# Kernel tuning notes

Hardware: AMD Instinct MI355X
Metric: run time of the kernel (lower is better)

The kernel has to match this reference:

```python
import jax, jax.numpy as jnp
import numpy as np

DIM = 1024
NUM_HEADS = 16
HEAD_DIM = DIM // NUM_HEADS


def _rope(x):
    # x: (B*H, L, hd). ESM-style rotary embedding with rotate_half.
    L, hd = x.shape[1], x.shape[2]
    inv_freq = 1.0 / (10000.0 ** (jnp.arange(0, hd, 2, dtype=jnp.float32) / hd))
    t = jnp.arange(L, dtype=jnp.float32)
    freqs = t[:, None] * inv_freq[None, :]          # (L, hd/2)
    emb = jnp.concatenate([freqs, freqs], axis=-1)   # (L, hd)
    cos, sin = jnp.cos(emb), jnp.sin(emb)
    x1, x2 = jnp.split(x, 2, axis=-1)
    rot = jnp.concatenate([-x2, x1], axis=-1)
    return x * cos + rot * sin


def setup_inputs() -> dict:
    key = jax.random.key(0)
    ks = jax.random.split(key, 10)
    L, N, D = 2048, 1, DIM
    query = jax.random.normal(ks[0], (L, N, D), dtype=jnp.float32)
    asym_ids = jnp.sort(jax.random.randint(ks[1], (N, L), 0, 4), axis=-1)
    s = 0.02
    wq = s * jax.random.normal(ks[2], (D, D), dtype=jnp.float32)
    wk = s * jax.random.normal(ks[3], (D, D), dtype=jnp.float32)
    wv = s * jax.random.normal(ks[4], (D, D), dtype=jnp.float32)
    wo = s * jax.random.normal(ks[5], (D, D), dtype=jnp.float32)
    bq = s * jax.random.normal(ks[6], (D,), dtype=jnp.float32)
    bk = s * jax.random.normal(ks[7], (D,), dtype=jnp.float32)
    bv = s * jax.random.normal(ks[8], (D,), dtype=jnp.float32)
    bo = s * jax.random.normal(ks[9], (D,), dtype=jnp.float32)
    return {"query": query, "asym_ids": asym_ids, "wq": wq, "bq": bq,
            "wk": wk, "bk": bk, "wv": wv, "bv": bv, "wo": wo, "bo": bo}


def reference(query, asym_ids, wq, bq, wk, bk, wv, bv, wo, bo):
    L, N, D = query.shape
    H, hd = NUM_HEADS, HEAD_DIM
    scaling = 1.0 / np.sqrt(hd)

    q = (query @ wq.T + bq) * scaling
    k = query @ wk.T + bk
    v = query @ wv.T + bv

    def to_bh(x):  # (L, N, D) -> (N*H, L, hd)
        return x.reshape(L, N * H, hd).transpose(1, 0, 2)

    q, k, v = to_bh(q), to_bh(k), to_bh(v)

    # raw scores (pre-RoPE), rpe scores (post-RoPE)
    raw = jnp.einsum('ble,bme->blm', q, k).reshape(N, H, L, L)
    qr, kr = _rope(q), _rope(k)
    rpe = jnp.einsum('ble,bme->blm', qr, kr).reshape(N, H, L, L)

    avg = jnp.mean(rpe - raw, axis=(0, 1), keepdims=True)          # (1,1,L,L)
    asym_mask = asym_ids[:, :, None] == asym_ids[:, None, :]        # (N,L,L)
    attn_weights = jnp.where(asym_mask[:, None], rpe, raw + avg)    # (N,H,L,L)

    probs = jax.nn.softmax(attn_weights, axis=-1)
    attn = jnp.einsum('nhlm,nhme->nhle', probs, v.reshape(N, H, L, hd))
    attn = attn.transpose(2, 0, 1, 3).reshape(L, N, D)
    out = attn @ wo.T + bo
    attn_weights_avg = jnp.mean(probs, axis=1)  # (N, L, L)
    return out, attn_weights_avg
```

## Files before the change

### kernel.cpp

```cpp
#include <hip/hip_runtime.h>

#define L 2048
#define D 1024
#define NH 16
#define HD 64
#define SPLIT 4
#define JCH (L / SPLIT)
#define LOG2E 1.4426950408889634f

typedef __attribute__((ext_vector_type(8))) short bf16x8;
typedef __attribute__((ext_vector_type(4))) float f32x4;

#define MFMA(a, b, c) __builtin_amdgcn_mfma_f32_16x16x32_bf16(a, b, c, 0, 0, 0)

__device__ __forceinline__ short f2bf(float x) {
  unsigned u = __float_as_uint(x);
  u = (u + 0x7FFFu + ((u >> 16) & 1u)) >> 16;
  return (short)u;
}

__device__ __forceinline__ void gll16(const void* g, void* l) {
  __builtin_amdgcn_global_load_lds(
      (const __attribute__((address_space(1))) void*)(uintptr_t)g,
      (__attribute__((address_space(3))) void*)(unsigned)(uintptr_t)l, 16, 0, 0);
}

__global__ void trig_kernel(float* __restrict__ costab, float* __restrict__ sintab) {
  int idx = blockIdx.x * blockDim.x + threadIdx.x;
  int t = idx >> 5, fi = idx & 31;
  float f = exp2f(-(float)fi * (13.287712379549449f / 32.0f));
  float ang = (float)t * f;
  costab[idx] = cosf(ang);
  sintab[idx] = sinf(ang);
}

__global__ void f2bf4_kernel(const float* __restrict__ in, short* __restrict__ out, int n4) {
  int i = blockIdx.x * blockDim.x + threadIdx.x;
  if (i < n4) {
    float4 v = ((const float4*)in)[i];
    short4 o;
    o.x = f2bf(v.x); o.y = f2bf(v.y); o.z = f2bf(v.z); o.w = f2bf(v.w);
    ((short4*)out)[i] = o;
  }
}

__global__ __launch_bounds__(256) void proj_kernel(
    const short* __restrict__ X, const short* __restrict__ W,
    const float* __restrict__ bias, const float* __restrict__ costab,
    const float* __restrict__ sintab, int mode,
    short* __restrict__ out_main, short* __restrict__ out_rope) {
  int w = threadIdx.x >> 6, lane = threadIdx.x & 63;
  int c = lane & 15, g = lane >> 4;
  int wi0 = blockIdx.y * 128 + (w >> 1) * 64;
  int wj0 = blockIdx.x * 128 + (w & 1) * 64;

  f32x4 acc[4][4];
#pragma unroll
  for (int m = 0; m < 4; ++m)
#pragma unroll
    for (int n = 0; n < 4; ++n) acc[m][n] = (f32x4){0.f, 0.f, 0.f, 0.f};

  for (int k0 = 0; k0 < D; k0 += 32) {
    bf16x8 aF[4], bF[4];
#pragma unroll
    for (int m = 0; m < 4; ++m)
      aF[m] = *(const bf16x8*)(X + (size_t)(wi0 + m * 16 + c) * D + k0 + g * 8);
#pragma unroll
    for (int n = 0; n < 4; ++n)
      bF[n] = *(const bf16x8*)(W + (size_t)(wj0 + n * 16 + c) * D + k0 + g * 8);
#pragma unroll
    for (int m = 0; m < 4; ++m)
#pragma unroll
      for (int n = 0; n < 4; ++n) acc[m][n] = MFMA(aF[m], bF[n], acc[m][n]);
  }

  float scale = (mode == 0) ? 0.125f : 1.0f;
#pragma unroll
  for (int m = 0; m < 4; ++m) {
#pragma unroll
    for (int r = 0; r < 4; ++r) {
      int i = wi0 + m * 16 + g * 4 + r;
      float v4[4];
#pragma unroll
      for (int n = 0; n < 4; ++n)
        v4[n] = (acc[m][n][r] + bias[wj0 + n * 16 + c]) * scale;
      if (mode == 2) {
#pragma unroll
        for (int n = 0; n < 4; ++n) {
          int col = wj0 + n * 16 + c;
          out_main[(size_t)col * L + i] = f2bf(v4[n]);
        }
      } else {
#pragma unroll
        for (int n = 0; n < 4; ++n) {
          int col = wj0 + n * 16 + c;
          out_main[(size_t)i * D + col] = f2bf(v4[n]);
          float rot = (n < 2) ? -v4[n + 2] : v4[n - 2];
          int fidx = i * 32 + (n & 1) * 16 + c;
          float vr = v4[n] * costab[fidx] + rot * sintab[fidx];
          out_rope[(size_t)i * D + col] = f2bf(vr);
        }
      }
    }
  }
}

__global__ __launch_bounds__(256) void avg_kernel(
    const short* __restrict__ QR, const short* __restrict__ KR,
    const short* __restrict__ Qs, const short* __restrict__ Kb,
    f32x4* __restrict__ avg4) {
  int w = threadIdx.x >> 6, lane = threadIdx.x & 63;
  int c = lane & 15, g = lane >> 4;
  int wi0 = blockIdx.y * 128 + (w >> 1) * 64;
  int wj0 = blockIdx.x * 128 + (w & 1) * 64;

  f32x4 acc1[4][4], acc2[4][4];
#pragma unroll
  for (int m = 0; m < 4; ++m)
#pragma unroll
    for (int n = 0; n < 4; ++n) {
      acc1[m][n] = (f32x4){0.f, 0.f, 0.f, 0.f};
      acc2[m][n] = (f32x4){0.f, 0.f, 0.f, 0.f};
    }

  for (int k0 = 0; k0 < D; k0 += 32) {
    bf16x8 aF[4], bF[4], a2F[4], b2F[4];
#pragma unroll
    for (int m = 0; m < 4; ++m) {
      aF[m] = *(const bf16x8*)(QR + (size_t)(wi0 + m * 16 + c) * D + k0 + g * 8);
      a2F[m] = *(const bf16x8*)(Qs + (size_t)(wi0 + m * 16 + c) * D + k0 + g * 8);
    }
#pragma unroll
    for (int n = 0; n < 4; ++n) {
      bF[n] = *(const bf16x8*)(KR + (size_t)(wj0 + n * 16 + c) * D + k0 + g * 8);
      b2F[n] = *(const bf16x8*)(Kb + (size_t)(wj0 + n * 16 + c) * D + k0 + g * 8);
    }
#pragma unroll
    for (int m = 0; m < 4; ++m)
#pragma unroll
      for (int n = 0; n < 4; ++n) {
        acc1[m][n] = MFMA(aF[m], bF[n], acc1[m][n]);
        acc2[m][n] = MFMA(a2F[m], b2F[n], acc2[m][n]);
      }
  }

#pragma unroll
  for (int m = 0; m < 4; ++m)
#pragma unroll
    for (int n = 0; n < 4; ++n) {
      int j = wj0 + n * 16 + c;
      f32x4 o;
#pragma unroll
      for (int r = 0; r < 4; ++r) o[r] = (acc1[m][n][r] - acc2[m][n][r]) * 0.0625f;
      avg4[(size_t)(((wi0 + m * 16) >> 2) + g) * L + j] = o;
    }
}

__global__ __launch_bounds__(256) void flash3_kernel(
    const short* __restrict__ Qs, const short* __restrict__ Kb,
    const short* __restrict__ QR, const short* __restrict__ KR,
    const short* __restrict__ Vt, const f32x4* __restrict__ avg4,
    const int* __restrict__ ids, float* __restrict__ m_part,
    float* __restrict__ l_part, float* __restrict__ acc_part) {
  int h = blockIdx.y, sp = blockIdx.z;
  int w = threadIdx.x >> 6, lane = threadIdx.x & 63;
  int c = lane & 15, g = lane >> 4;
  int i0 = blockIdx.x * 64 + w * 16;
  int hk = h * 64;

  __shared__ short kb_lds[2][64 * 64];
  __shared__ short kr_lds[2][64 * 64];
  __shared__ short plds[4][16][72];

  int srow = lane >> 3;
  int sxor = (lane & 7) ^ srow;
  int r0a = w * 16, r0b = w * 16 + 8;

  bf16x8 qA[2], qrA[2];
  {
    const short* qp = Qs + (size_t)(i0 + c) * D + hk + g * 8;
    const short* qrp = QR + (size_t)(i0 + c) * D + hk + g * 8;
    qA[0] = *(const bf16x8*)qp;   qA[1] = *(const bf16x8*)(qp + 32);
    qrA[0] = *(const bf16x8*)qrp; qrA[1] = *(const bf16x8*)(qrp + 32);
  }

  int idi[4];
  float mrun[4], lsum[4];
  f32x4 acc[4];
#pragma unroll
  for (int r = 0; r < 4; ++r) {
    idi[r] = ids[i0 + g * 4 + r];
    mrun[r] = -3.0e38f;
    lsum[r] = 0.f;
  }
#pragma unroll
  for (int n = 0; n < 4; ++n) acc[n] = (f32x4){0.f, 0.f, 0.f, 0.f};

  const f32x4* avrow = avg4 + (size_t)((i0 >> 2) + g) * L;
  int jbase = sp * JCH;
  const int NT = JCH / 64;

  gll16(Kb + (size_t)(jbase + r0a + srow) * D + hk + sxor * 8, &kb_lds[0][r0a * 64]);
  gll16(Kb + (size_t)(jbase + r0b + srow) * D + hk + sxor * 8, &kb_lds[0][r0b * 64]);
  gll16(KR + (size_t)(jbase + r0a + srow) * D + hk + sxor * 8, &kr_lds[0][r0a * 64]);
  gll16(KR + (size_t)(jbase + r0b + srow) * D + hk + sxor * 8, &kr_lds[0][r0b * 64]);

  f32x4 avn[4];
  int idjn[4];
#pragma unroll
  for (int sub = 0; sub < 4; ++sub) {
    avn[sub] = avrow[jbase + sub * 16 + c];
    idjn[sub] = ids[jbase + sub * 16 + c];
  }
  __syncthreads();

  int cur = 0;
  for (int jt = 0; jt < NT; ++jt) {
    int jb = jbase + jt * 64;

    if (jt + 1 < NT) {
      int jn = jb + 64;
      short* kd = &kb_lds[cur ^ 1][0];
      short* rd = &kr_lds[cur ^ 1][0];
      gll16(Kb + (size_t)(jn + r0a + srow) * D + hk + sxor * 8, kd + r0a * 64);
      gll16(Kb + (size_t)(jn + r0b + srow) * D + hk + sxor * 8, kd + r0b * 64);
      gll16(KR + (size_t)(jn + r0a + srow) * D + hk + sxor * 8, rd + r0a * 64);
      gll16(KR + (size_t)(jn + r0b + srow) * D + hk + sxor * 8, rd + r0b * 64);
    }

    bf16x8 vf0[4], vf1[4];
#pragma unroll
    for (int n = 0; n < 4; ++n) {
      const short* vp = Vt + (size_t)(hk + n * 16 + c) * L + jb + g * 8;
      vf0[n] = *(const bf16x8*)vp;
      vf1[n] = *(const bf16x8*)(vp + 32);
    }

    f32x4 av[4];
    int idj[4];
#pragma unroll
    for (int sub = 0; sub < 4; ++sub) { av[sub] = avn[sub]; idj[sub] = idjn[sub]; }
    if (jt + 1 < NT) {
#pragma unroll
      for (int sub = 0; sub < 4; ++sub) {
        avn[sub] = avrow[jb + 64 + sub * 16 + c];
        idjn[sub] = ids[jb + 64 + sub * 16 + c];
      }
    }

    const short* kbb = &kb_lds[cur][c * 64];
    const short* krb = &kr_lds[cur][c * 64];
    int co0 = (g ^ (c & 7)) * 8;
    int co1 = ((4 + g) ^ (c & 7)) * 8;
    f32x4 raw[4], rpe[4];
#pragma unroll
    for (int sub = 0; sub < 4; ++sub) {
      bf16x8 k0 = *(const bf16x8*)(kbb + sub * 1024 + co0);
      bf16x8 k1 = *(const bf16x8*)(kbb + sub * 1024 + co1);
      bf16x8 kr0 = *(const bf16x8*)(krb + sub * 1024 + co0);
      bf16x8 kr1 = *(const bf16x8*)(krb + sub * 1024 + co1);
      f32x4 z = (f32x4){0.f, 0.f, 0.f, 0.f};
      raw[sub] = MFMA(qA[1], k1, MFMA(qA[0], k0, z));
      rpe[sub] = MFMA(qrA[1], kr1, MFMA(qrA[0], kr0, z));
    }

    float t[4][4];
#pragma unroll
    for (int sub = 0; sub < 4; ++sub)
#pragma unroll
      for (int r = 0; r < 4; ++r) {
        float sv = (idi[r] == idj[sub]) ? rpe[sub][r] : (raw[sub][r] + av[sub][r]);
        t[sub][r] = sv * LOG2E;
      }

    float tm[4];
#pragma unroll
    for (int r = 0; r < 4; ++r)
      tm[r] = fmaxf(fmaxf(t[0][r], t[1][r]), fmaxf(t[2][r], t[3][r]));
    bool ok = (tm[0] <= mrun[0] + 8.f) && (tm[1] <= mrun[1] + 8.f) &&
              (tm[2] <= mrun[2] + 8.f) && (tm[3] <= mrun[3] + 8.f);
    if (!__all(ok)) {
#pragma unroll
      for (int r = 0; r < 4; ++r) {
        float m2 = tm[r];
#pragma unroll
        for (int d = 1; d < 16; d <<= 1) m2 = fmaxf(m2, __shfl_xor(m2, d));
        float mn = fmaxf(mrun[r], m2);
        float so = exp2f(mrun[r] - mn);
        mrun[r] = mn;
        lsum[r] *= so;
#pragma unroll
        for (int n = 0; n < 4; ++n) acc[n][r] *= so;
      }
    }

#pragma unroll
    for (int sub = 0; sub < 4; ++sub)
#pragma unroll
      for (int r = 0; r < 4; ++r) {
        float p = exp2f(t[sub][r] - mrun[r]);
        lsum[r] += p;
        plds[w][g * 4 + r][sub * 16 + c] = f2bf(p);
      }

    {
      bf16x8 pa = *(const bf16x8*)(&plds[w][c][g * 8]);
#pragma unroll
      for (int n = 0; n < 4; ++n) acc[n] = MFMA(pa, vf0[n], acc[n]);
      bf16x8 pb = *(const bf16x8*)(&plds[w][c][32 + g * 8]);
#pragma unroll
      for (int n = 0; n < 4; ++n) acc[n] = MFMA(pb, vf1[n], acc[n]);
    }

    __syncthreads();
    cur ^= 1;
  }

#pragma unroll
  for (int r = 0; r < 4; ++r) {
#pragma unroll
    for (int d = 1; d < 16; d <<= 1) lsum[r] += __shfl_xor(lsum[r], d);
  }
  size_t sb = (size_t)(sp * NH + h) * L;
  if (c == 0) {
#pragma unroll
    for (int r = 0; r < 4; ++r) {
      m_part[sb + i0 + g * 4 + r] = mrun[r];
      l_part[sb + i0 + g * 4 + r] = lsum[r];
    }
  }
#pragma unroll
  for (int n = 0; n < 4; ++n)
#pragma unroll
    for (int r = 0; r < 4; ++r)
      acc_part[(sb + i0 + g * 4 + r) * HD + n * 16 + c] = acc[n][r];
}

__global__ void merge_kernel(const float* __restrict__ m_part,
                             const float* __restrict__ l_part,
                             const float* __restrict__ acc_part,
                             float* __restrict__ mfin, float* __restrict__ lfin,
                             short* __restrict__ attn_bf) {
  int idx = blockIdx.x * 256 + threadIdx.x;
  int d = idx & (HD - 1);
  int hi = idx >> 6;
  int i = hi & (L - 1), h = hi >> 11;
  float m4 = -3.0e38f;
#pragma unroll
  for (int s = 0; s < SPLIT; ++s)
    m4 = fmaxf(m4, m_part[(size_t)(s * NH + h) * L + i]);
  float l = 0.f, o = 0.f;
#pragma unroll
  for (int s = 0; s < SPLIT; ++s) {
    size_t sb = (size_t)(s * NH + h) * L + i;
    float e = exp2f(m_part[sb] - m4);
    l += l_part[sb] * e;
    o += acc_part[sb * HD + d] * e;
  }
  attn_bf[(size_t)i * D + h * HD + d] = f2bf(o / l);
  if (d == 0) { mfin[h * L + i] = m4; lfin[h * L + i] = l; }
}

__global__ __launch_bounds__(256) void pavg_kernel(
    const short* __restrict__ Qs, const short* __restrict__ Kb,
    const short* __restrict__ QR, const short* __restrict__ KR,
    const f32x4* __restrict__ avg4, const int* __restrict__ ids,
    const float* __restrict__ m_ws, const float* __restrict__ l_ws,
    float* __restrict__ out1) {
  int j0 = blockIdx.x * 64;
  int iblk = blockIdx.y * 64;
  int w = threadIdx.x >> 6, lane = threadIdx.x & 63;
  int c = lane & 15, g = lane >> 4;
  int i0 = iblk + w * 16;

  __shared__ short kb_lds[2][64 * 64];
  __shared__ short kr_lds[2][64 * 64];
  __shared__ float mS[NH][64], lS[NH][64];

  int srow = lane >> 3;
  int sxor = (lane & 7) ^ srow;
  int r0a = w * 16, r0b = w * 16 + 8;

  for (int idx = threadIdx.x; idx < NH * 64; idx += 256) {
    int hh = idx >> 6, rr = idx & 63;
    mS[hh][rr] = m_ws[hh * L + iblk + rr];
    lS[hh][rr] = 1.0f / l_ws[hh * L + iblk + rr];
  }

  gll16(Kb + (size_t)(j0 + r0a + srow) * D + sxor * 8, &kb_lds[0][r0a * 64]);
  gll16(Kb + (size_t)(j0 + r0b + srow) * D + sxor * 8, &kb_lds[0][r0b * 64]);
  gll16(KR + (size_t)(j0 + r0a + srow) * D + sxor * 8, &kr_lds[0][r0a * 64]);
  gll16(KR + (size_t)(j0 + r0b + srow) * D + sxor * 8, &kr_lds[0][r0b * 64]);

  int idi[4], idj[4];
  f32x4 av[4];
  {
    const f32x4* avrow = avg4 + (size_t)((i0 >> 2) + g) * L;
#pragma unroll
    for (int sub = 0; sub < 4; ++sub) {
      av[sub] = avrow[j0 + sub * 16 + c];
      idj[sub] = ids[j0 + sub * 16 + c];
    }
#pragma unroll
    for (int r = 0; r < 4; ++r) idi[r] = ids[i0 + g * 4 + r];
  }

  f32x4 psum[4];
#pragma unroll
  for (int sub = 0; sub < 4; ++sub) psum[sub] = (f32x4){0.f, 0.f, 0.f, 0.f};

  const short* qbase = Qs + (size_t)(i0 + c) * D + g * 8;
  const short* qrbase = QR + (size_t)(i0 + c) * D + g * 8;

  bf16x8 nq0 = *(const bf16x8*)qbase, nq1 = *(const bf16x8*)(qbase + 32);
  bf16x8 nqr0 = *(const bf16x8*)qrbase, nqr1 = *(const bf16x8*)(qrbase + 32);

  __syncthreads();

  int cur = 0;
#pragma unroll 1
  for (int hh = 0; hh < NH; ++hh) {
    if (hh + 1 < NH) {
      int hkn = (hh + 1) * 64;
      short* kd = &kb_lds[cur ^ 1][0];
      short* rd = &kr_lds[cur ^ 1][0];
      gll16(Kb + (size_t)(j0 + r0a + srow) * D + hkn + sxor * 8, kd + r0a * 64);
      gll16(Kb + (size_t)(j0 + r0b + srow) * D + hkn + sxor * 8, kd + r0b * 64);
      gll16(KR + (size_t)(j0 + r0a + srow) * D + hkn + sxor * 8, rd + r0a * 64);
      gll16(KR + (size_t)(j0 + r0b + srow) * D + hkn + sxor * 8, rd + r0b * 64);
    }

    bf16x8 q0 = nq0, q1 = nq1, qr0 = nqr0, qr1 = nqr1;
    if (hh + 1 < NH) {
      int hkn = (hh + 1) * 64;
      nq0 = *(const bf16x8*)(qbase + hkn);
      nq1 = *(const bf16x8*)(qbase + hkn + 32);
      nqr0 = *(const bf16x8*)(qrbase + hkn);
      nqr1 = *(const bf16x8*)(qrbase + hkn + 32);
    }

    const short* kbb = &kb_lds[cur][c * 64];
    const short* krb = &kr_lds[cur][c * 64];
    int co0 = (g ^ (c & 7)) * 8;
    int co1 = ((4 + g) ^ (c & 7)) * 8;
    f32x4 raw[4], rpe[4];
#pragma unroll
    for (int sub = 0; sub < 4; ++sub) {
      bf16x8 k0 = *(const bf16x8*)(kbb + sub * 1024 + co0);
      bf16x8 k1 = *(const bf16x8*)(kbb + sub * 1024 + co1);
      bf16x8 kr0 = *(const bf16x8*)(krb + sub * 1024 + co0);
      bf16x8 kr1 = *(const bf16x8*)(krb + sub * 1024 + co1);
      f32x4 z = (f32x4){0.f, 0.f, 0.f, 0.f};
      raw[sub] = MFMA(q1, k1, MFMA(q0, k0, z));
      rpe[sub] = MFMA(qr1, kr1, MFMA(qr0, kr0, z));
    }

    f32x4 m4 = *(const f32x4*)(&mS[hh][w * 16 + g * 4]);
    f32x4 l4 = *(const f32x4*)(&lS[hh][w * 16 + g * 4]);
#pragma unroll
    for (int sub = 0; sub < 4; ++sub)
#pragma unroll
      for (int r = 0; r < 4; ++r) {
        float s = (idi[r] == idj[sub]) ? rpe[sub][r] : (raw[sub][r] + av[sub][r]);
        psum[sub][r] += exp2f(s * LOG2E - m4[r]) * l4[r];
      }

    __syncthreads();
    cur ^= 1;
  }

#pragma unroll
  for (int sub = 0; sub < 4; ++sub)
#pragma unroll
    for (int r = 0; r < 4; ++r)
      out1[(size_t)(i0 + g * 4 + r) * L + j0 + sub * 16 + c] = psum[sub][r] * 0.0625f;
}

__global__ __launch_bounds__(256) void outproj_kernel(
    const short* __restrict__ A, const short* __restrict__ W,
    const float* __restrict__ bias, float* __restrict__ out) {
  int w = threadIdx.x >> 6, lane = threadIdx.x & 63;
  int c = lane & 15, g = lane >> 4;
  int wi0 = blockIdx.y * 128 + (w >> 1) * 64;
  int wj0 = blockIdx.x * 128 + (w & 1) * 64;

  f32x4 acc[4][4];
#pragma unroll
  for (int m = 0; m < 4; ++m)
#pragma unroll
    for (int n = 0; n < 4; ++n) acc[m][n] = (f32x4){0.f, 0.f, 0.f, 0.f};

  for (int k0 = 0; k0 < D; k0 += 32) {
    bf16x8 aF[4], bF[4];
#pragma unroll
    for (int m = 0; m < 4; ++m)
      aF[m] = *(const bf16x8*)(A + (size_t)(wi0 + m * 16 + c) * D + k0 + g * 8);
#pragma unroll
    for (int n = 0; n < 4; ++n)
      bF[n] = *(const bf16x8*)(W + (size_t)(wj0 + n * 16 + c) * D + k0 + g * 8);
#pragma unroll
    for (int m = 0; m < 4; ++m)
#pragma unroll
      for (int n = 0; n < 4; ++n) acc[m][n] = MFMA(aF[m], bF[n], acc[m][n]);
  }

#pragma unroll
  for (int m = 0; m < 4; ++m)
#pragma unroll
    for (int n = 0; n < 4; ++n)
#pragma unroll
      for (int r = 0; r < 4; ++r) {
        int i = wi0 + m * 16 + g * 4 + r;
        int col = wj0 + n * 16 + c;
        out[(size_t)i * D + col] = acc[m][n][r] + bias[col];
      }
}

extern "C" void kernel_launch(void* const* d_in, const int* in_sizes, int n_in,
                              void* d_out, int out_size, void* d_ws, size_t ws_size,
                              hipStream_t stream) {
  const float* query = (const float*)d_in[0];
  const int* ids = (const int*)d_in[1];
  const float* wq = (const float*)d_in[2];
  const float* bq = (const float*)d_in[3];
  const float* wk = (const float*)d_in[4];
  const float* bk = (const float*)d_in[5];
  const float* wv = (const float*)d_in[6];
  const float* bv = (const float*)d_in[7];
  const float* wo = (const float*)d_in[8];
  const float* bo = (const float*)d_in[9];

  char* p = (char*)d_ws;
  auto carve = [&](size_t bytes) {
    char* r = p;
    p += (bytes + 255) & ~(size_t)255;
    return r;
  };
  short* Xbf = (short*)carve((size_t)L * D * 2);
  short* Wqb = (short*)carve((size_t)D * D * 2);
  short* Wkb = (short*)carve((size_t)D * D * 2);
  short* Wvb = (short*)carve((size_t)D * D * 2);
  short* Wob = (short*)carve((size_t)D * D * 2);
  short* Qs = (short*)carve((size_t)L * D * 2);
  short* QRb = (short*)carve((size_t)L * D * 2);
  short* Kbb = (short*)carve((size_t)L * D * 2);
  short* KRb = (short*)carve((size_t)L * D * 2);
  short* Vt = (short*)carve((size_t)L * D * 2);
  f32x4* avg4 = (f32x4*)carve((size_t)L * L * 4);
  float* m_ws = (float*)carve((size_t)NH * L * 4);
  float* l_ws = (float*)carve((size_t)NH * L * 4);
  short* attn_bf = (short*)carve((size_t)L * D * 2);
  float* costab = (float*)carve((size_t)L * 32 * 4);
  float* sintab = (float*)carve((size_t)L * 32 * 4);
  float* m_part = (float*)carve((size_t)SPLIT * NH * L * 4);
  float* l_part = (float*)carve((size_t)SPLIT * NH * L * 4);
  float* acc_part = (float*)carve((size_t)SPLIT * NH * L * HD * 4);

  float* out0 = (float*)d_out;
  float* out1 = out0 + (size_t)L * D;

  trig_kernel<<<(L * 32) / 256, 256, 0, stream>>>(costab, sintab);

  f2bf4_kernel<<<(L * D / 4 + 255) / 256, 256, 0, stream>>>(query, Xbf, L * D / 4);
  f2bf4_kernel<<<(D * D / 4 + 255) / 256, 256, 0, stream>>>(wq, Wqb, D * D / 4);
  f2bf4_kernel<<<(D * D / 4 + 255) / 256, 256, 0, stream>>>(wk, Wkb, D * D / 4);
  f2bf4_kernel<<<(D * D / 4 + 255) / 256, 256, 0, stream>>>(wv, Wvb, D * D / 4);
  f2bf4_kernel<<<(D * D / 4 + 255) / 256, 256, 0, stream>>>(wo, Wob, D * D / 4);

  dim3 gproj(D / 128, L / 128);
  proj_kernel<<<gproj, 256, 0, stream>>>(Xbf, Wqb, bq, costab, sintab, 0, Qs, QRb);
  proj_kernel<<<gproj, 256, 0, stream>>>(Xbf, Wkb, bk, costab, sintab, 1, Kbb, KRb);
  proj_kernel<<<gproj, 256, 0, stream>>>(Xbf, Wvb, bv, costab, sintab, 2, Vt, nullptr);

  avg_kernel<<<dim3(L / 128, L / 128), 256, 0, stream>>>(QRb, KRb, Qs, Kbb, avg4);

  flash3_kernel<<<dim3(L / 64, NH, SPLIT), 256, 0, stream>>>(
      Qs, Kbb, QRb, KRb, Vt, avg4, ids, m_part, l_part, acc_part);

  merge_kernel<<<(NH * L * HD) / 256, 256, 0, stream>>>(m_part, l_part, acc_part,
                                                        m_ws, l_ws, attn_bf);

  pavg_kernel<<<dim3(L / 64, L / 64), 256, 0, stream>>>(Qs, Kbb, QRb, KRb, avg4, ids,
                                                        m_ws, l_ws, out1);

  outproj_kernel<<<dim3(D / 128, L / 128), 256, 0, stream>>>(attn_bf, Wob, bo, out0);
}
```

Before: 402.7 us.

## Skip unused raw/RoPE score MFMAs for uniform-id tiles and fold log2e into Q

Adds per-wave and per-block checks for whether the query and key tiles each carry a single asym id. When they do, the flash and probability-average kernels compute only the score that will be selected (the RoPE score for matching ids, the raw score plus avg otherwise) and skip the other MFMAs, LDS reads and K/Q loads. The log2e factor is folded into the Q projection scale so the per-element multiply is dropped. The P staging buffer changes from padded rows to an XOR swizzle, and occupancy hints are added to launch bounds. This relies on the uniform-id check being correct for sorted ids. The folded log2e must also be applied consistently in the avg kernel and in QR.

Measured after the change: 582.4 us. +44.6%, slower.

```diff
diff --git a/kernel.cpp b/kernel.cpp
--- a/kernel.cpp
+++ b/kernel.cpp
@@ -74,7 +74,7 @@
       for (int n = 0; n < 4; ++n) acc[m][n] = MFMA(aF[m], bF[n], acc[m][n]);
   }
 
-  float scale = (mode == 0) ? 0.125f : 1.0f;
+  float scale = (mode == 0) ? 0.125f * LOG2E : 1.0f;
 #pragma unroll
   for (int m = 0; m < 4; ++m) {
 #pragma unroll
@@ -156,7 +156,7 @@
     }
 }
 
-__global__ __launch_bounds__(256) void flash3_kernel(
+__global__ __launch_bounds__(256, 4) void flash3_kernel(
     const short* __restrict__ Qs, const short* __restrict__ Kb,
     const short* __restrict__ QR, const short* __restrict__ KR,
     const short* __restrict__ Vt, const f32x4* __restrict__ avg4,
@@ -170,7 +170,7 @@
 
   __shared__ short kb_lds[2][64 * 64];
   __shared__ short kr_lds[2][64 * 64];
-  __shared__ short plds[4][16][72];
+  __shared__ short plds[4][16][64];
 
   int srow = lane >> 3;
   int sxor = (lane & 7) ^ srow;
@@ -195,6 +195,10 @@
   }
 #pragma unroll
   for (int n = 0; n < 4; ++n) acc[n] = (f32x4){0.f, 0.f, 0.f, 0.f};
+
+  int ifirst = __shfl(idi[0], 0);
+  bool iu = __all((idi[0] == idi[1]) & (idi[1] == idi[2]) & (idi[2] == idi[3]) &
+                  (idi[0] == ifirst));
 
   const f32x4* avrow = avg4 + (size_t)((i0 >> 2) + g) * L;
   int jbase = sp * JCH;
@@ -248,30 +252,51 @@
       }
     }
 
+    int jfirst = __shfl(idj[0], 0);
+    bool ju = __all((idj[0] == idj[1]) & (idj[1] == idj[2]) & (idj[2] == idj[3]) &
+                    (idj[0] == jfirst));
+
     const short* kbb = &kb_lds[cur][c * 64];
     const short* krb = &kr_lds[cur][c * 64];
     int co0 = (g ^ (c & 7)) * 8;
     int co1 = ((4 + g) ^ (c & 7)) * 8;
-    f32x4 raw[4], rpe[4];
-#pragma unroll
-    for (int sub = 0; sub < 4; ++sub) {
-      bf16x8 k0 = *(const bf16x8*)(kbb + sub * 1024 + co0);
-      bf16x8 k1 = *(const bf16x8*)(kbb + sub * 1024 + co1);
-      bf16x8 kr0 = *(const bf16x8*)(krb + sub * 1024 + co0);
-      bf16x8 kr1 = *(const bf16x8*)(krb + sub * 1024 + co1);
-      f32x4 z = (f32x4){0.f, 0.f, 0.f, 0.f};
-      raw[sub] = MFMA(qA[1], k1, MFMA(qA[0], k0, z));
-      rpe[sub] = MFMA(qrA[1], kr1, MFMA(qrA[0], kr0, z));
-    }
 
     float t[4][4];
-#pragma unroll
-    for (int sub = 0; sub < 4; ++sub)
-#pragma unroll
-      for (int r = 0; r < 4; ++r) {
-        float sv = (idi[r] == idj[sub]) ? rpe[sub][r] : (raw[sub][r] + av[sub][r]);
-        t[sub][r] = sv * LOG2E;
-      }
+    if (iu && ju && ifirst == jfirst) {
+#pragma unroll
+      for (int sub = 0; sub < 4; ++sub) {
+        bf16x8 kr0 = *(const bf16x8*)(krb + sub * 1024 + co0);
+        bf16x8 kr1 = *(const bf16x8*)(krb + sub * 1024 + co1);
+        f32x4 z = (f32x4){0.f, 0.f, 0.f, 0.f};
+        f32x4 rp = MFMA(qrA[1], kr1, MFMA(qrA[0], kr0, z));
+#pragma unroll
+        for (int r = 0; r < 4; ++r) t[sub][r] = rp[r];
+      }
+    } else if (iu && ju) {
+#pragma unroll
+      for (int sub = 0; sub < 4; ++sub) {
+        bf16x8 k0 = *(const bf16x8*)(kbb + sub * 1024 + co0);
+        bf16x8 k1 = *(const bf16x8*)(kbb + sub * 1024 + co1);
+        f32x4 z = (f32x4){0.f, 0.f, 0.f, 0.f};
+        f32x4 rw = MFMA(qA[1], k1, MFMA(qA[0], k0, z));
+#pragma unroll
+        for (int r = 0; r < 4; ++r) t[sub][r] = rw[r] + av[sub][r];
+      }
+    } else {
+#pragma unroll
+      for (int sub = 0; sub < 4; ++sub) {
+        bf16x8 k0 = *(const bf16x8*)(kbb + sub * 1024 + co0);
+        bf16x8 k1 = *(const bf16x8*)(kbb + sub * 1024 + co1);
+        bf16x8 kr0 = *(const bf16x8*)(krb + sub * 1024 + co0);
+        bf16x8 kr1 = *(const bf16x8*)(krb + sub * 1024 + co1);
+        f32x4 z = (f32x4){0.f, 0.f, 0.f, 0.f};
+        f32x4 rw = MFMA(qA[1], k1, MFMA(qA[0], k0, z));
+        f32x4 rp = MFMA(qrA[1], kr1, MFMA(qrA[0], kr0, z));
+#pragma unroll
+        for (int r = 0; r < 4; ++r)
+          t[sub][r] = (idi[r] == idj[sub]) ? rp[r] : (rw[r] + av[sub][r]);
+      }
+    }
 
     float tm[4];
 #pragma unroll
@@ -300,14 +325,17 @@
       for (int r = 0; r < 4; ++r) {
         float p = exp2f(t[sub][r] - mrun[r]);
         lsum[r] += p;
-        plds[w][g * 4 + r][sub * 16 + c] = f2bf(p);
+        int prow = g * 4 + r;
+        plds[w][prow][(sub * 16 + c) ^ ((prow & 7) << 3)] = f2bf(p);
       }
 
     {
-      bf16x8 pa = *(const bf16x8*)(&plds[w][c][g * 8]);
+      int pc0 = (g * 8) ^ ((c & 7) << 3);
+      int pc1 = (32 + g * 8) ^ ((c & 7) << 3);
+      bf16x8 pa = *(const bf16x8*)(&plds[w][c][pc0]);
 #pragma unroll
       for (int n = 0; n < 4; ++n) acc[n] = MFMA(pa, vf0[n], acc[n]);
-      bf16x8 pb = *(const bf16x8*)(&plds[w][c][32 + g * 8]);
+      bf16x8 pb = *(const bf16x8*)(&plds[w][c][pc1]);
 #pragma unroll
       for (int n = 0; n < 4; ++n) acc[n] = MFMA(pb, vf1[n], acc[n]);
     }
@@ -361,7 +389,7 @@
   if (d == 0) { mfin[h * L + i] = m4; lfin[h * L + i] = l; }
 }
 
-__global__ __launch_bounds__(256) void pavg_kernel(
+__global__ __launch_bounds__(256, 4) void pavg_kernel(
     const short* __restrict__ Qs, const short* __restrict__ Kb,
     const short* __restrict__ QR, const short* __restrict__ KR,
     const f32x4* __restrict__ avg4, const int* __restrict__ ids,
@@ -381,16 +409,24 @@
   int sxor = (lane & 7) ^ srow;
   int r0a = w * 16, r0b = w * 16 + 8;
 
+  int si0 = ids[iblk], si1 = ids[iblk + 63];
+  int sj0 = ids[j0], sj1 = ids[j0 + 63];
+  int mode = (si0 == si1 && sj0 == sj1) ? ((si0 == sj0) ? 0 : 1) : 2;
+
   for (int idx = threadIdx.x; idx < NH * 64; idx += 256) {
     int hh = idx >> 6, rr = idx & 63;
     mS[hh][rr] = m_ws[hh * L + iblk + rr];
     lS[hh][rr] = 1.0f / l_ws[hh * L + iblk + rr];
   }
 
-  gll16(Kb + (size_t)(j0 + r0a + srow) * D + sxor * 8, &kb_lds[0][r0a * 64]);
-  gll16(Kb + (size_t)(j0 + r0b + srow) * D + sxor * 8, &kb_lds[0][r0b * 64]);
-  gll16(KR + (size_t)(j0 + r0a + srow) * D + sxor * 8, &kr_lds[0][r0a * 64]);
-  gll16(KR + (size_t)(j0 + r0b + srow) * D + sxor * 8, &kr_lds[0][r0b * 64]);
+  if (mode != 0) {
+    gll16(Kb + (size_t)(j0 + r0a + srow) * D + sxor * 8, &kb_lds[0][r0a * 64]);
+    gll16(Kb + (size_t)(j0 + r0b + srow) * D + sxor * 8, &kb_lds[0][r0b * 64]);
+  }
+  if (mode != 1) {
+    gll16(KR + (size_t)(j0 + r0a + srow) * D + sxor * 8, &kr_lds[0][r0a * 64]);
+    gll16(KR + (size_t)(j0 + r0b + srow) * D + sxor * 8, &kr_lds[0][r0b * 64]);
+  }
 
   int idi[4], idj[4];
   f32x4 av[4];
@@ -412,8 +448,9 @@
   const short* qbase = Qs + (size_t)(i0 + c) * D + g * 8;
   const short* qrbase = QR + (size_t)(i0 + c) * D + g * 8;
 
-  bf16x8 nq0 = *(const bf16x8*)qbase, nq1 = *(const bf16x8*)(qbase + 32);
-  bf16x8 nqr0 = *(const bf16x8*)qrbase, nqr1 = *(const bf16x8*)(qrbase + 32);
+  bf16x8 nq0, nq1, nqr0, nqr1;
+  if (mode != 0) { nq0 = *(const bf16x8*)qbase; nq1 = *(const bf16x8*)(qbase + 32); }
+  if (mode != 1) { nqr0 = *(const bf16x8*)qrbase; nqr1 = *(const bf16x8*)(qrbase + 32); }
 
   __syncthreads();
 
@@ -424,46 +461,76 @@
       int hkn = (hh + 1) * 64;
       short* kd = &kb_lds[cur ^ 1][0];
       short* rd = &kr_lds[cur ^ 1][0];
-      gll16(Kb + (size_t)(j0 + r0a + srow) * D + hkn + sxor * 8, kd + r0a * 64);
-      gll16(Kb + (size_t)(j0 + r0b + srow) * D + hkn + sxor * 8, kd + r0b * 64);
-      gll16(KR + (size_t)(j0 + r0a + srow) * D + hkn + sxor * 8, rd + r0a * 64);
-      gll16(KR + (size_t)(j0 + r0b + srow) * D + hkn + sxor * 8, rd + r0b * 64);
+      if (mode != 0) {
+        gll16(Kb + (size_t)(j0 + r0a + srow) * D + hkn + sxor * 8, kd + r0a * 64);
+        gll16(Kb + (size_t)(j0 + r0b + srow) * D + hkn + sxor * 8, kd + r0b * 64);
+      }
+      if (mode != 1) {
+        gll16(KR + (size_t)(j0 + r0a + srow) * D + hkn + sxor * 8, rd + r0a * 64);
+        gll16(KR + (size_t)(j0 + r0b + srow) * D + hkn + sxor * 8, rd + r0b * 64);
+      }
     }
 
     bf16x8 q0 = nq0, q1 = nq1, qr0 = nqr0, qr1 = nqr1;
     if (hh + 1 < NH) {
       int hkn = (hh + 1) * 64;
-      nq0 = *(const bf16x8*)(qbase + hkn);
-      nq1 = *(const bf16x8*)(qbase + hkn + 32);
-      nqr0 = *(const bf16x8*)(qrbase + hkn);
-      nqr1 = *(const bf16x8*)(qrbase + hkn + 32);
+      if (mode != 0) {
+        nq0 = *(const bf16x8*)(qbase + hkn);
+        nq1 = *(const bf16x8*)(qbase + hkn + 32);
+      }
+      if (mode != 1) {
+        nqr0 = *(const bf16x8*)(qrbase + hkn);
+        nqr1 = *(const bf16x8*)(qrbase + hkn + 32);
+      }
     }
 
     const short* kbb = &kb_lds[cur][c * 64];
     const short* krb = &kr_lds[cur][c * 64];
     int co0 = (g ^ (c & 7)) * 8;
     int co1 = ((4 + g) ^ (c & 7)) * 8;
-    f32x4 raw[4], rpe[4];
-#pragma unroll
-    for (int sub = 0; sub < 4; ++sub) {
-      bf16x8 k0 = *(const bf16x8*)(kbb + sub * 1024 + co0);
-      bf16x8 k1 = *(const bf16x8*)(kbb + sub * 1024 + co1);
-      bf16x8 kr0 = *(const bf16x8*)(krb + sub * 1024 + co0);
-      bf16x8 kr1 = *(const bf16x8*)(krb + sub * 1024 + co1);
-      f32x4 z = (f32x4){0.f, 0.f, 0.f, 0.f};
-      raw[sub] = MFMA(q1, k1, MFMA(q0, k0, z));
-      rpe[sub] = MFMA(qr1, kr1, MFMA(qr0, kr0, z));
-    }
 
     f32x4 m4 = *(const f32x4*)(&mS[hh][w * 16 + g * 4]);
     f32x4 l4 = *(const f32x4*)(&lS[hh][w * 16 + g * 4]);
-#pragma unroll
-    for (int sub = 0; sub < 4; ++sub)
-#pragma unroll
-      for (int r = 0; r < 4; ++r) {
-        float s = (idi[r] == idj[sub]) ? rpe[sub][r] : (raw[sub][r] + av[sub][r]);
-        psum[sub][r] += exp2f(s * LOG2E - m4[r]) * l4[r];
-      }
+
+    if (mode == 0) {
+#pragma unroll
+      for (int sub = 0; sub < 4; ++sub) {
+        bf16x8 kr0 = *(const bf16x8*)(krb + sub * 1024 + co0);
+        bf16x8 kr1 = *(const bf16x8*)(krb + sub * 1024 + co1);
+        f32x4 z = (f32x4){0.f, 0.f, 0.f, 0.f};
+        f32x4 rp = MFMA(qr1, kr1, MFMA(qr0, kr0, z));
+#pragma unroll
+        for (int r = 0; r < 4; ++r)
+          psum[sub][r] += exp2f(rp[r] - m4[r]) * l4[r];
+      }
+    } else if (mode == 1) {
+#pragma unroll
+      for (int sub = 0; sub < 4; ++sub) {
+        bf16x8 k0 = *(const bf16x8*)(kbb + sub * 1024 + co0);
+        bf16x8 k1 = *(const bf16x8*)(kbb + sub * 1024 + co1);
+        f32x4 z = (f32x4){0.f, 0.f, 0.f, 0.f};
+        f32x4 rw = MFMA(q1, k1, MFMA(q0, k0, z));
+#pragma unroll
+        for (int r = 0; r < 4; ++r)
+          psum[sub][r] += exp2f(rw[r] + av[sub][r] - m4[r]) * l4[r];
+      }
+    } else {
+#pragma unroll
+      for (int sub = 0; sub < 4; ++sub) {
+        bf16x8 k0 = *(const bf16x8*)(kbb + sub * 1024 + co0);
+        bf16x8 k1 = *(const bf16x8*)(kbb + sub * 1024 + co1);
+        bf16x8 kr0 = *(const bf16x8*)(krb + sub * 1024 + co0);
+        bf16x8 kr1 = *(const bf16x8*)(krb + sub * 1024 + co1);
+        f32x4 z = (f32x4){0.f, 0.f, 0.f, 0.f};
+        f32x4 rw = MFMA(q1, k1, MFMA(q0, k0, z));
+        f32x4 rp = MFMA(qr1, kr1, MFMA(qr0, kr0, z));
+#pragma unroll
+        for (int r = 0; r < 4; ++r) {
+          float s = (idi[r] == idj[sub]) ? rp[r] : (rw[r] + av[sub][r]);
+          psum[sub][r] += exp2f(s - m4[r]) * l4[r];
+        }
+      }
+    }
 
     __syncthreads();
     cur ^= 1;
```
